# Optimization experiments

Hardware: AMD Instinct MI355X
Metric: run time of the kernel (lower is better)

The kernel has to match this reference:

```python
import jax, jax.numpy as jnp
import numpy as np

# ---- instant-ngp style multi-resolution hash-grid config (matches torch-ngp HashEncoder) ----
NUM_LEVELS = 16
LEVEL_DIM = 2
BASE_RES = 16
DESIRED_RES = 2048
LOG2_T = 19
T_MAX = 2 ** LOG2_T
_pls = np.exp2(np.log2(DESIRED_RES / BASE_RES) / (NUM_LEVELS - 1))  # per-level scale ~1.3819
RESOLUTIONS = [int(np.ceil(BASE_RES * _pls ** l)) for l in range(NUM_LEVELS)]
LEVEL_SIZES = [min(T_MAX, int(np.ceil((r + 1) ** 3 / 8) * 8)) for r in RESOLUTIONS]
OFFSETS = np.concatenate([[0], np.cumsum(LEVEL_SIZES)]).astype(np.int64)
TOTAL_PARAMS = int(OFFSETS[-1])
HASHED = [(r + 1) ** 3 > T_MAX for r in RESOLUTIONS]
CORNERS = np.array([[i, j, k] for i in (0, 1) for j in (0, 1) for k in (0, 1)], dtype=np.float32)  # [8,3]

N_POINTS = 524288
MULTIRES = 6  # positional embedding freqs -> input_ch = 3 + 3*2*6 = 39
D_IN0 = 3 + MULTIRES * 6 + NUM_LEVELS * LEVEL_DIM  # 71


def hash_encode(x, table):
    """x: [N,3] in [0,1]; table: [TOTAL_PARAMS, LEVEL_DIM] -> [N, NUM_LEVELS*LEVEL_DIM]."""
    cn = jnp.asarray(CORNERS)              # [8,3]
    cn_u = cn.astype(jnp.uint32)
    p1, p2, p3 = jnp.uint32(1), jnp.uint32(2654435761), jnp.uint32(805459861)
    outs = []
    for l in range(NUM_LEVELS):
        res = RESOLUTIONS[l]
        pos = x * jnp.float32(res - 1)     # [N,3]
        p0 = jnp.floor(pos)
        w = pos - p0                        # [N,3] trilinear fractions
        cpos = p0.astype(jnp.uint32)[:, None, :] + cn_u[None]  # [N,8,3] corner coords
        if HASHED[l]:
            idx = (cpos[..., 0] * p1) ^ (cpos[..., 1] * p2) ^ (cpos[..., 2] * p3)
            idx = (idx % jnp.uint32(LEVEL_SIZES[l])).astype(jnp.int32)
        else:
            stride = jnp.uint32(res + 1)
            idx = (cpos[..., 0] + cpos[..., 1] * stride + cpos[..., 2] * stride * stride).astype(jnp.int32)
        feats = table[int(OFFSETS[l]) + idx]  # [N,8,LEVEL_DIM] irregular gather
        cw = jnp.where(cn[None] == 1.0, w[:, None, :], 1.0 - w[:, None, :])  # [N,8,3]
        wgt = cw[..., 0] * cw[..., 1] * cw[..., 2]  # [N,8]
        outs.append(jnp.einsum('nc,ncd->nd', wgt, feats))  # [N,LEVEL_DIM]
    return jnp.concatenate(outs, axis=-1)


def pos_embed(x):
    # NeRF embedder, include_input=True, log-sampled freqs 2^0..2^(MULTIRES-1), sin/cos
    freqs = jnp.asarray(2.0 ** np.arange(MULTIRES), dtype=x.dtype)   # [6]
    ang = x[:, None, :] * freqs[None, :, None]                        # [N,6,3]
    sc = jnp.stack([jnp.sin(ang), jnp.cos(ang)], axis=2)              # [N,6,2,3]
    return jnp.concatenate([x, sc.reshape(x.shape[0], -1)], axis=-1)  # [N,39]


def linear_wn(x, v, g, b):
    # nn.utils.weight_norm: W = g * v / ||v||_row
    Wn = v * (g / jnp.linalg.norm(v, axis=1))[:, None]
    return x @ Wn.T + b


def softplus100(x):
    # nn.Softplus(beta=100)
    return jax.nn.softplus(100.0 * x) * 0.01


def setup_inputs() -> dict:
    key = jax.random.key(0)
    ks = jax.random.split(key, 8)
    x = jax.random.uniform(ks[0], (N_POINTS, 3), dtype=jnp.float32)
    hash_table = jax.random.uniform(ks[1], (TOTAL_PARAMS, LEVEL_DIM), jnp.float32, -1e-4, 1e-4)

    def lin(k, dout, din):
        v = jax.random.normal(k, (dout, din), jnp.float32) * jnp.float32(np.sqrt(2.0 / dout))
        g = jnp.linalg.norm(v, axis=1)  # weight_norm init: g = ||v||
        b = jnp.zeros((dout,), jnp.float32)
        return v, g, b

    v0, g0, b0 = lin(ks[2], 256, D_IN0)   # 71 -> 256
    v1, g1, b1 = lin(ks[3], 256, 256)     # 256 -> 256
    v2, g2, b2 = lin(ks[4], 257, 256)     # 256 -> 1 + feature_vector_size
    return {"x": x, "hash_table": hash_table,
            "v0": v0, "g0": g0, "b0": b0,
            "v1": v1, "g1": g1, "b1": b1,
            "v2": v2, "g2": g2, "b2": b2}


def reference(x, hash_table, v0, g0, b0, v1, g1, b1, v2, g2, b2):
    # ImplicitNetworkGrid.forward (divide_factor = 1.0, use_grid_feature = True)
    feat = hash_encode(x, hash_table)                    # [N,32]
    h = jnp.concatenate([pos_embed(x), feat], axis=-1)   # [N,71] = cat(embed, feature)
    h = softplus100(linear_wn(h, v0, g0, b0))
    h = softplus100(linear_wn(h, v1, g1, b1))
    return linear_wn(h, v2, g2, b2)                      # [N,257]: sdf + feature vector
```

## Files before the change

### kernel.cpp

```cpp
#include <hip/hip_runtime.h>
#include <cmath>

typedef float f32x4 __attribute__((ext_vector_type(4)));
typedef short short8 __attribute__((ext_vector_type(8)));

#define N_POINTS 524288
#define TMASK 0x7FFFFu

struct HashCfg { int res[16]; int off[16]; unsigned hashed_mask; int total; };

#define S0_OFF   0
#define S1_OFF   1024
#define S2_OFF   2048
#define W2L_OFF  3328
#define B0_OFF   4608
#define B1_OFF   (B0_OFF + 49152)
#define B2_OFF   (B1_OFF + 131072)
#define TBF_OFF  (B2_OFF + 131072)

__device__ inline unsigned short f2bf(float f){
  unsigned u = __float_as_uint(f);
  u = (u + 0x7FFFu + ((u >> 16) & 1u)) >> 16;
  return (unsigned short)u;
}
__device__ inline float bf2f(unsigned short h){
  return __uint_as_float(((unsigned)h) << 16);
}
__device__ inline float softplus100_fast(float x){
  float y = 100.f * x;
  return 0.01f * (fmaxf(y, 0.f) + __logf(1.f + __expf(-fabsf(y))));
}

__global__ void scale_kernel(const float* __restrict__ v0, const float* __restrict__ g0,
                             const float* __restrict__ v1, const float* __restrict__ g1,
                             const float* __restrict__ v2, const float* __restrict__ g2,
                             char* __restrict__ ws){
  int r = blockIdx.x * 256 + threadIdx.x;
  if (r < 256){
    float s = 0.f;
    for (int k = 0; k < 71; k++){ float t = v0[r*71+k]; s += t*t; }
    ((float*)(ws + S0_OFF))[r] = g0[r] / sqrtf(s);
  } else if (r < 512){
    int o = r - 256; float s = 0.f;
    for (int k = 0; k < 256; k++){ float t = v1[o*256+k]; s += t*t; }
    ((float*)(ws + S1_OFF))[o] = g1[o] / sqrtf(s);
  } else if (r < 769){
    int o = r - 512; float s = 0.f;
    for (int k = 0; k < 256; k++){ float t = v2[o*256+k]; s += t*t; }
    ((float*)(ws + S2_OFF))[o] = g2[o] / sqrtf(s);
  }
}

__global__ void pack_kernel(const float* __restrict__ v0, const float* __restrict__ v1,
                            const float* __restrict__ v2, char* __restrict__ ws){
  int i = blockIdx.x * 256 + threadIdx.x;
  const float* s0 = (const float*)(ws + S0_OFF);
  const float* s1 = (const float*)(ws + S1_OFF);
  const float* s2 = (const float*)(ws + S2_OFF);
  if (i < 24576){
    int j = i & 7, l = (i >> 3) & 63, q = i >> 9;
    int kt = q % 3, nt = q / 3;
    int k = kt*32 + (l >> 4)*8 + j, col = nt*16 + (l & 15);
    float v = (k < 71) ? v0[col*71 + k] * s0[col] : 0.f;
    ((unsigned short*)(ws + B0_OFF))[i] = f2bf(v);
  } else if (i < 90112){
    int e = i - 24576;
    int j = e & 7, l = (e >> 3) & 63, q = e >> 9;
    int kt = q & 7, nt = q >> 3;
    int k = kt*32 + (l >> 4)*8 + j, col = nt*16 + (l & 15);
    ((unsigned short*)(ws + B1_OFF))[e] = f2bf(v1[col*256 + k] * s1[col]);
  } else if (i < 155648){
    int e = i - 90112;
    int j = e & 7, l = (e >> 3) & 63, q = e >> 9;
    int kt = q & 7, nt = q >> 3;
    int k = kt*32 + (l >> 4)*8 + j, col = nt*16 + (l & 15);
    ((unsigned short*)(ws + B2_OFF))[e] = f2bf(v2[col*256 + k] * s2[col]);
  } else if (i < 155904){
    int k = i - 155648;
    ((float*)(ws + W2L_OFF))[k] = v2[256*256 + k] * s2[256];
  }
}

__global__ void tconv_kernel(const float* __restrict__ table, char* __restrict__ ws, int total){
  int i = blockIdx.x * 256 + threadIdx.x;
  if (i < total){
    float2 v = ((const float2*)table)[i];
    unsigned lo = ((unsigned)f2bf(v.x));
    unsigned hi = ((unsigned)f2bf(v.y)) << 16;
    ((unsigned*)(ws + TBF_OFF))[i] = lo | hi;
  }
}

template<int USEBF>
__global__ __launch_bounds__(256, 4) void fused2(
    const float* __restrict__ xin, const float* __restrict__ table,
    char* __restrict__ ws,
    const float* __restrict__ b0, const float* __restrict__ b1, const float* __restrict__ b2,
    float* __restrict__ out, HashCfg cfg)
{
  __shared__ unsigned short buf[64 * 256];
  __shared__ float colsc[4][64];

  const int tid = threadIdx.x;
  const int p   = tid & 63;
  const int grp = tid >> 6;
  const int gp  = blockIdx.x * 64 + p;

  const float x0 = xin[gp*3], x1 = xin[gp*3+1], x2 = xin[gp*3+2];
  const unsigned* __restrict__ tbf = (const unsigned*)(ws + TBF_OFF);

  auto stB = [&](int row, int col, float v){
    buf[row*256 + (col ^ ((row & 7) << 3))] = f2bf(v);
  };
  auto ldB = [&](int row, int kb) -> short8 {
    return *(const short8*)&buf[row*256 + (kb ^ ((row & 7) << 3))];
  };

  {
    float wxa[4], wya[4], wza[4];
    unsigned vb[2][8];
    float2   vf2[2][8];

    auto issue_level = [&](int ii, int slot){
      int lev = grp*4 + ii;
      int res = cfg.res[lev];
      float scl = (float)(res - 1);
      float px = x0*scl, py = x1*scl, pz = x2*scl;
      float fx = floorf(px), fy = floorf(py), fz = floorf(pz);
      wxa[ii] = px - fx; wya[ii] = py - fy; wza[ii] = pz - fz;
      unsigned cx0 = (unsigned)fx, cy0 = (unsigned)fy, cz0 = (unsigned)fz;
      unsigned r1 = (unsigned)(res + 1);
      bool hl = (cfg.hashed_mask >> lev) & 1;
      unsigned base = (unsigned)cfg.off[lev];
      #pragma unroll
      for (int c = 0; c < 8; c++){
        unsigned bx = (c >> 2) & 1, by = (c >> 1) & 1, bz = c & 1;
        unsigned cx = cx0 + bx, cy = cy0 + by, cz = cz0 + bz;
        unsigned idx = hl ? ((cx ^ (cy * 2654435761u) ^ (cz * 805459861u)) & TMASK)
                          : (cx + cy * r1 + cz * r1 * r1);
        if (USEBF) vb[slot][c]  = tbf[base + idx];
        else       vf2[slot][c] = *(const float2*)(table + (size_t)(base + idx) * 2u);
      }
    };
    auto consume_level = [&](int ii, int slot){
      int lev = grp*4 + ii;
      float wx = wxa[ii], wy = wya[ii], wz = wza[ii];
      float f0 = 0.f, f1 = 0.f;
      #pragma unroll
      for (int c = 0; c < 8; c++){
        unsigned bx = (c >> 2) & 1, by = (c >> 1) & 1, bz = c & 1;
        float w = (bx ? wx : 1.f - wx) * (by ? wy : 1.f - wy) * (bz ? wz : 1.f - wz);
        if (USEBF){
          unsigned u = vb[slot][c];
          f0 += w * __uint_as_float(u << 16);
          f1 += w * __uint_as_float(u & 0xffff0000u);
        } else {
          f0 += w * vf2[slot][c].x;
          f1 += w * vf2[slot][c].y;
        }
      }
      stB(p, 39 + 2*lev, f0);
      stB(p, 40 + 2*lev, f1);
    };

    issue_level(0, 0); issue_level(1, 1);

    if (grp < 3){
      float xv[3] = {x0, x1, x2};
      #pragma unroll
      for (int fi = 0; fi < 2; fi++){
        int f = grp*2 + fi;
        float fr = (float)(1 << f);
        #pragma unroll
        for (int d = 0; d < 3; d++){
          float a = xv[d] * fr;
          stB(p, 3 + f*6 + d,     __sinf(a));
          stB(p, 3 + f*6 + 3 + d, __cosf(a));
        }
      }
    } else {
      stB(p, 0, x0); stB(p, 1, x1); stB(p, 2, x2);
      #pragma unroll
      for (int c = 71; c < 96; c++)
        buf[p*256 + (c ^ ((p & 7) << 3))] = 0;
    }

    consume_level(0, 0); consume_level(1, 1);
    issue_level(2, 0);   issue_level(3, 1);
    consume_level(2, 0); consume_level(3, 1);
  }
  __syncthreads();

  const int l  = tid & 63;
  const int lr = l & 15;
  const int lh = l >> 4;
  const int wv = grp;
  const short8* B0p = (const short8*)(ws + B0_OFF);
  const short8* B1p = (const short8*)(ws + B1_OFF);
  const short8* B2p = (const short8*)(ws + B2_OFF);

  {
    f32x4 acc[4][4];
    #pragma unroll
    for (int a = 0; a < 4; a++)
      #pragma unroll
      for (int b = 0; b < 4; b++) acc[a][b] = (f32x4){0.f,0.f,0.f,0.f};
    #pragma unroll
    for (int kt = 0; kt < 3; kt++){
      short8 af[4];
      #pragma unroll
      for (int mt = 0; mt < 4; mt++) af[mt] = ldB(mt*16 + lr, kt*32 + lh*8);
      #pragma unroll
      for (int nt = 0; nt < 4; nt++){
        short8 bf = B0p[((wv*4 + nt)*3 + kt)*64 + l];
        #pragma unroll
        for (int mt = 0; mt < 4; mt++)
          acc[mt][nt] = __builtin_amdgcn_mfma_f32_16x16x32_bf16(af[mt], bf, acc[mt][nt], 0, 0, 0);
      }
    }
    __syncthreads();
    float bb[4];
    #pragma unroll
    for (int nt = 0; nt < 4; nt++) bb[nt] = b0[wv*64 + nt*16 + lr];
    #pragma unroll
    for (int mt = 0; mt < 4; mt++)
      #pragma unroll
      for (int nt = 0; nt < 4; nt++){
        int c = wv*64 + nt*16 + lr;
        #pragma unroll
        for (int j = 0; j < 4; j++)
          stB(mt*16 + lh*4 + j, c, softplus100_fast(acc[mt][nt][j] + bb[nt]));
      }
  }
  __syncthreads();

  {
    f32x4 acc[4][4];
    #pragma unroll
    for (int a = 0; a < 4; a++)
      #pragma unroll
      for (int b = 0; b < 4; b++) acc[a][b] = (f32x4){0.f,0.f,0.f,0.f};
    #pragma unroll
    for (int kt = 0; kt < 8; kt++){
      short8 af[4];
      #pragma unroll
      for (int mt = 0; mt < 4; mt++) af[mt] = ldB(mt*16 + lr, kt*32 + lh*8);
      #pragma unroll
      for (int nt = 0; nt < 4; nt++){
        short8 bf = B1p[((wv*4 + nt)*8 + kt)*64 + l];
        #pragma unroll
        for (int mt = 0; mt < 4; mt++)
          acc[mt][nt] = __builtin_amdgcn_mfma_f32_16x16x32_bf16(af[mt], bf, acc[mt][nt], 0, 0, 0);
      }
    }
    __syncthreads();
    float bb[4];
    #pragma unroll
    for (int nt = 0; nt < 4; nt++) bb[nt] = b1[wv*64 + nt*16 + lr];
    #pragma unroll
    for (int mt = 0; mt < 4; mt++)
      #pragma unroll
      for (int nt = 0; nt < 4; nt++){
        int c = wv*64 + nt*16 + lr;
        #pragma unroll
        for (int j = 0; j < 4; j++)
          stB(mt*16 + lh*4 + j, c, softplus100_fast(acc[mt][nt][j] + bb[nt]));
      }
  }
  __syncthreads();

  {
    const float* w2l = (const float*)(ws + W2L_OFF);
    float s = 0.f;
    #pragma unroll
    for (int q = 0; q < 8; q++){
      short8 h = ldB(l, wv*64 + q*8);
      #pragma unroll
      for (int j = 0; j < 8; j++)
        s += bf2f((unsigned short)h[j]) * w2l[wv*64 + q*8 + j];
    }
    colsc[wv][l] = s;
  }

  {
    f32x4 acc[4][4];
    #pragma unroll
    for (int a = 0; a < 4; a++)
      #pragma unroll
      for (int b = 0; b < 4; b++) acc[a][b] = (f32x4){0.f,0.f,0.f,0.f};
    #pragma unroll
    for (int kt = 0; kt < 8; kt++){
      short8 af[4];
      #pragma unroll
      for (int mt = 0; mt < 4; mt++) af[mt] = ldB(mt*16 + lr, kt*32 + lh*8);
      #pragma unroll
      for (int nt = 0; nt < 4; nt++){
        short8 bf = B2p[((wv*4 + nt)*8 + kt)*64 + l];
        #pragma unroll
        for (int mt = 0; mt < 4; mt++)
          acc[mt][nt] = __builtin_amdgcn_mfma_f32_16x16x32_bf16(af[mt], bf, acc[mt][nt], 0, 0, 0);
      }
    }
    float bb[4];
    #pragma unroll
    for (int nt = 0; nt < 4; nt++) bb[nt] = b2[wv*64 + nt*16 + lr];
    const float b2last = b2[256];

    float* st = (float*)buf;
    #pragma unroll
    for (int r16 = 0; r16 < 4; r16++){
      __syncthreads();
      #pragma unroll
      for (int nt = 0; nt < 4; nt++){
        int c = wv*64 + nt*16 + lr;
        #pragma unroll
        for (int j = 0; j < 4; j++)
          st[(lh*4 + j)*257 + c] = acc[r16][nt][j] + bb[nt];
      }
      if (tid < 16){
        int gr = r16*16 + tid;
        st[tid*257 + 256] = colsc[0][gr] + colsc[1][gr] + colsc[2][gr] + colsc[3][gr] + b2last;
      }
      __syncthreads();
      float4* dst4 = (float4*)(out + (size_t)(blockIdx.x*64 + r16*16) * 257);
      const float4* src4 = (const float4*)st;
      #pragma unroll 5
      for (int i = tid; i < 1028; i += 256) dst4[i] = src4[i];
    }
  }
}

static HashCfg make_cfg(){
  HashCfg c;
  double pls = exp2(log2(2048.0 / 16.0) / 15.0);
  long long off = 0;
  unsigned mask = 0;
  for (int l = 0; l < 16; l++){
    int r = (int)ceil(16.0 * pow(pls, (double)l));
    c.res[l] = r;
    c.off[l] = (int)off;
    double n3 = (double)(r + 1) * (double)(r + 1) * (double)(r + 1);
    long long size;
    if (n3 > 524288.0){ mask |= (1u << l); }
    size = (long long)(ceil(n3 / 8.0) * 8.0);
    if (size > 524288) size = 524288;
    off += size;
  }
  c.hashed_mask = mask;
  c.total = (int)off;
  return c;
}

extern "C" void kernel_launch(void* const* d_in, const int* in_sizes, int n_in,
                              void* d_out, int out_size, void* d_ws, size_t ws_size,
                              hipStream_t stream) {
  const float* x     = (const float*)d_in[0];
  const float* table = (const float*)d_in[1];
  const float* v0 = (const float*)d_in[2];
  const float* g0 = (const float*)d_in[3];
  const float* b0 = (const float*)d_in[4];
  const float* v1 = (const float*)d_in[5];
  const float* g1 = (const float*)d_in[6];
  const float* b1 = (const float*)d_in[7];
  const float* v2 = (const float*)d_in[8];
  const float* g2 = (const float*)d_in[9];
  const float* b2 = (const float*)d_in[10];
  float* out = (float*)d_out;
  char* ws = (char*)d_ws;

  HashCfg cfg = make_cfg();
  size_t ws_need_bf = (size_t)TBF_OFF + (size_t)cfg.total * 4u;

  hipLaunchKernelGGL(scale_kernel, dim3(4), dim3(256), 0, stream, v0, g0, v1, g1, v2, g2, ws);
  hipLaunchKernelGGL(pack_kernel, dim3(609), dim3(256), 0, stream, v0, v1, v2, ws);

  if (ws_size >= ws_need_bf){
    hipLaunchKernelGGL(tconv_kernel, dim3((cfg.total + 255) / 256), dim3(256), 0, stream,
                       table, ws, cfg.total);
    hipLaunchKernelGGL((fused2<1>), dim3(N_POINTS / 64), dim3(256), 0, stream,
                       x, table, ws, b0, b1, b2, out, cfg);
  } else {
    hipLaunchKernelGGL((fused2<0>), dim3(N_POINTS / 64), dim3(256), 0, stream,
                       x, table, ws, b0, b1, b2, out, cfg);
  }
}
```

Measured before the change: 870.2 us.

## Sort points by Morton cell before fused hash-grid MLP to improve gather locality

Adds a counting sort of points by a 32^3 Morton-coded cell (histogram, single-block scan, atomic scatter), so each block processes spatially nearby points. The goal is better cache reuse in the hash-table gathers. Blocks are remapped with an XCD-style swizzle, and all four levels' gathers are now issued before any are consumed. The output is written directly to permuted rows instead of being staged through shared memory for coalesced float4 stores. The trade-offs are three extra kernels plus a memset, uncoalesced scattered output writes of 257-float rows, and more registers held live for the gathers.

```diff
diff --git a/kernel.cpp b/kernel.cpp
--- a/kernel.cpp
+++ b/kernel.cpp
@@ -6,6 +6,7 @@
 
 #define N_POINTS 524288
 #define TMASK 0x7FFFFu
+#define NCELLS 32768
 
 struct HashCfg { int res[16]; int off[16]; unsigned hashed_mask; int total; };
 
@@ -29,6 +30,16 @@
 __device__ inline float softplus100_fast(float x){
   float y = 100.f * x;
   return 0.01f * (fmaxf(y, 0.f) + __logf(1.f + __expf(-fabsf(y))));
+}
+__device__ inline unsigned morton5(unsigned cx, unsigned cy, unsigned cz){
+  unsigned k = 0;
+  #pragma unroll
+  for (int b = 0; b < 5; b++){
+    k |= ((cx >> b) & 1u) << (3*b)
+       | ((cy >> b) & 1u) << (3*b + 1)
+       | ((cz >> b) & 1u) << (3*b + 2);
+  }
+  return k;
 }
 
 __global__ void scale_kernel(const float* __restrict__ v0, const float* __restrict__ g0,
@@ -91,22 +102,66 @@
   }
 }
 
+__global__ void hist_kernel(const float* __restrict__ xin,
+                            unsigned* __restrict__ hist, unsigned* __restrict__ keys){
+  int i = blockIdx.x * 256 + threadIdx.x;
+  float x0 = xin[i*3], x1 = xin[i*3+1], x2 = xin[i*3+2];
+  unsigned cx = min(31u, (unsigned)(x0 * 32.f));
+  unsigned cy = min(31u, (unsigned)(x1 * 32.f));
+  unsigned cz = min(31u, (unsigned)(x2 * 32.f));
+  unsigned k = morton5(cx, cy, cz);
+  keys[i] = k;
+  atomicAdd(&hist[k], 1u);
+}
+
+__global__ __launch_bounds__(1024) void scan_kernel(unsigned* __restrict__ hist){
+  __shared__ unsigned sdata[1024];
+  int t = threadIdx.x;
+  unsigned loc[32];
+  unsigned s = 0;
+  #pragma unroll
+  for (int k = 0; k < 32; k++){ loc[k] = hist[t*32 + k]; s += loc[k]; }
+  sdata[t] = s;
+  __syncthreads();
+  for (int d = 1; d < 1024; d <<= 1){
+    unsigned v = (t >= d) ? sdata[t - d] : 0u;
+    __syncthreads();
+    sdata[t] += v;
+    __syncthreads();
+  }
+  unsigned run = (t == 0) ? 0u : sdata[t - 1];
+  #pragma unroll
+  for (int k = 0; k < 32; k++){ unsigned c = loc[k]; hist[t*32 + k] = run; run += c; }
+}
+
+__global__ void scatter_kernel(const unsigned* __restrict__ keys,
+                               unsigned* __restrict__ hist, int* __restrict__ perm){
+  int i = blockIdx.x * 256 + threadIdx.x;
+  unsigned k = keys[i];
+  unsigned r = atomicAdd(&hist[k], 1u);
+  perm[r] = i;
+}
+
 template<int USEBF>
-__global__ __launch_bounds__(256, 4) void fused2(
+__global__ __launch_bounds__(256, 4) void fused3(
     const float* __restrict__ xin, const float* __restrict__ table,
-    char* __restrict__ ws,
+    char* __restrict__ ws, const int* __restrict__ perm,
     const float* __restrict__ b0, const float* __restrict__ b1, const float* __restrict__ b2,
     float* __restrict__ out, HashCfg cfg)
 {
   __shared__ unsigned short buf[64 * 256];
   __shared__ float colsc[4][64];
+  __shared__ int pids[64];
 
   const int tid = threadIdx.x;
   const int p   = tid & 63;
   const int grp = tid >> 6;
-  const int gp  = blockIdx.x * 64 + p;
-
-  const float x0 = xin[gp*3], x1 = xin[gp*3+1], x2 = xin[gp*3+2];
+  const int lb  = (blockIdx.x & 7) * 1024 + (blockIdx.x >> 3);
+  const int idx = lb * 64 + p;
+  const int pid = perm ? perm[idx] : idx;
+  if (grp == 0) pids[p] = pid;
+
+  const float x0 = xin[pid*3], x1 = xin[pid*3+1], x2 = xin[pid*3+2];
   const unsigned* __restrict__ tbf = (const unsigned*)(ws + TBF_OFF);
 
   auto stB = [&](int row, int col, float v){
@@ -118,10 +173,11 @@
 
   {
     float wxa[4], wya[4], wza[4];
-    unsigned vb[2][8];
-    float2   vf2[2][8];
-
-    auto issue_level = [&](int ii, int slot){
+    unsigned vb[4][8];
+    float2   vf2[4][8];
+
+    #pragma unroll
+    for (int ii = 0; ii < 4; ii++){
       int lev = grp*4 + ii;
       int res = cfg.res[lev];
       float scl = (float)(res - 1);
@@ -136,34 +192,12 @@
       for (int c = 0; c < 8; c++){
         unsigned bx = (c >> 2) & 1, by = (c >> 1) & 1, bz = c & 1;
         unsigned cx = cx0 + bx, cy = cy0 + by, cz = cz0 + bz;
-        unsigned idx = hl ? ((cx ^ (cy * 2654435761u) ^ (cz * 805459861u)) & TMASK)
-                          : (cx + cy * r1 + cz * r1 * r1);
-        if (USEBF) vb[slot][c]  = tbf[base + idx];
-        else       vf2[slot][c] = *(const float2*)(table + (size_t)(base + idx) * 2u);
-      }
-    };
-    auto consume_level = [&](int ii, int slot){
-      int lev = grp*4 + ii;
-      float wx = wxa[ii], wy = wya[ii], wz = wza[ii];
-      float f0 = 0.f, f1 = 0.f;
-      #pragma unroll
-      for (int c = 0; c < 8; c++){
-        unsigned bx = (c >> 2) & 1, by = (c >> 1) & 1, bz = c & 1;
-        float w = (bx ? wx : 1.f - wx) * (by ? wy : 1.f - wy) * (bz ? wz : 1.f - wz);
-        if (USEBF){
-          unsigned u = vb[slot][c];
-          f0 += w * __uint_as_float(u << 16);
-          f1 += w * __uint_as_float(u & 0xffff0000u);
-        } else {
-          f0 += w * vf2[slot][c].x;
-          f1 += w * vf2[slot][c].y;
-        }
-      }
-      stB(p, 39 + 2*lev, f0);
-      stB(p, 40 + 2*lev, f1);
-    };
-
-    issue_level(0, 0); issue_level(1, 1);
+        unsigned hidx = hl ? ((cx ^ (cy * 2654435761u) ^ (cz * 805459861u)) & TMASK)
+                           : (cx + cy * r1 + cz * r1 * r1);
+        if (USEBF) vb[ii][c]  = tbf[base + hidx];
+        else       vf2[ii][c] = *(const float2*)(table + (size_t)(base + hidx) * 2u);
+      }
+    }
 
     if (grp < 3){
       float xv[3] = {x0, x1, x2};
@@ -185,9 +219,27 @@
         buf[p*256 + (c ^ ((p & 7) << 3))] = 0;
     }
 
-    consume_level(0, 0); consume_level(1, 1);
-    issue_level(2, 0);   issue_level(3, 1);
-    consume_level(2, 0); consume_level(3, 1);
+    #pragma unroll
+    for (int ii = 0; ii < 4; ii++){
+      int lev = grp*4 + ii;
+      float wx = wxa[ii], wy = wya[ii], wz = wza[ii];
+      float f0 = 0.f, f1 = 0.f;
+      #pragma unroll
+      for (int c = 0; c < 8; c++){
+        unsigned bx = (c >> 2) & 1, by = (c >> 1) & 1, bz = c & 1;
+        float w = (bx ? wx : 1.f - wx) * (by ? wy : 1.f - wy) * (bz ? wz : 1.f - wz);
+        if (USEBF){
+          unsigned u = vb[ii][c];
+          f0 += w * __uint_as_float(u << 16);
+          f1 += w * __uint_as_float(u & 0xffff0000u);
+        } else {
+          f0 += w * vf2[ii][c].x;
+          f1 += w * vf2[ii][c].y;
+        }
+      }
+      stB(p, 39 + 2*lev, f0);
+      stB(p, 40 + 2*lev, f1);
+    }
   }
   __syncthreads();
 
@@ -301,32 +353,27 @@
           acc[mt][nt] = __builtin_amdgcn_mfma_f32_16x16x32_bf16(af[mt], bf, acc[mt][nt], 0, 0, 0);
       }
     }
+    __syncthreads();
     float bb[4];
     #pragma unroll
     for (int nt = 0; nt < 4; nt++) bb[nt] = b2[wv*64 + nt*16 + lr];
-    const float b2last = b2[256];
-
-    float* st = (float*)buf;
-    #pragma unroll
-    for (int r16 = 0; r16 < 4; r16++){
-      __syncthreads();
+    int rowid[4][4];
+    #pragma unroll
+    for (int mt = 0; mt < 4; mt++)
+      #pragma unroll
+      for (int j = 0; j < 4; j++) rowid[mt][j] = pids[mt*16 + lh*4 + j];
+    #pragma unroll
+    for (int mt = 0; mt < 4; mt++)
       #pragma unroll
       for (int nt = 0; nt < 4; nt++){
         int c = wv*64 + nt*16 + lr;
         #pragma unroll
         for (int j = 0; j < 4; j++)
-          st[(lh*4 + j)*257 + c] = acc[r16][nt][j] + bb[nt];
-      }
-      if (tid < 16){
-        int gr = r16*16 + tid;
-        st[tid*257 + 256] = colsc[0][gr] + colsc[1][gr] + colsc[2][gr] + colsc[3][gr] + b2last;
-      }
-      __syncthreads();
-      float4* dst4 = (float4*)(out + (size_t)(blockIdx.x*64 + r16*16) * 257);
-      const float4* src4 = (const float4*)st;
-      #pragma unroll 5
-      for (int i = tid; i < 1028; i += 256) dst4[i] = src4[i];
-    }
+          out[(size_t)rowid[mt][j]*257 + c] = acc[mt][nt][j] + bb[nt];
+      }
+    if (tid < 64)
+      out[(size_t)pids[tid]*257 + 256] =
+        colsc[0][tid] + colsc[1][tid] + colsc[2][tid] + colsc[3][tid] + b2[256];
   }
 }
 
@@ -369,18 +416,35 @@
   char* ws = (char*)d_ws;
 
   HashCfg cfg = make_cfg();
-  size_t ws_need_bf = (size_t)TBF_OFF + (size_t)cfg.total * 4u;
+  size_t tbf_bytes = (size_t)cfg.total * 4u;
+  size_t hist_off  = (TBF_OFF + tbf_bytes + 255) & ~(size_t)255;
+  size_t keys_off  = hist_off + (size_t)NCELLS * 4;
+  size_t perm_off  = keys_off + (size_t)N_POINTS * 4;
+  size_t need_sort = perm_off + (size_t)N_POINTS * 4;
+  size_t need_bf   = TBF_OFF + tbf_bytes;
 
   hipLaunchKernelGGL(scale_kernel, dim3(4), dim3(256), 0, stream, v0, g0, v1, g1, v2, g2, ws);
   hipLaunchKernelGGL(pack_kernel, dim3(609), dim3(256), 0, stream, v0, v1, v2, ws);
 
-  if (ws_size >= ws_need_bf){
+  if (ws_size >= need_sort){
+    unsigned* hist = (unsigned*)(ws + hist_off);
+    unsigned* keys = (unsigned*)(ws + keys_off);
+    int*      perm = (int*)(ws + perm_off);
+    hipMemsetAsync(hist, 0, (size_t)NCELLS * 4, stream);
     hipLaunchKernelGGL(tconv_kernel, dim3((cfg.total + 255) / 256), dim3(256), 0, stream,
                        table, ws, cfg.total);
-    hipLaunchKernelGGL((fused2<1>), dim3(N_POINTS / 64), dim3(256), 0, stream,
-                       x, table, ws, b0, b1, b2, out, cfg);
+    hipLaunchKernelGGL(hist_kernel, dim3(N_POINTS / 256), dim3(256), 0, stream, x, hist, keys);
+    hipLaunchKernelGGL(scan_kernel, dim3(1), dim3(1024), 0, stream, hist);
+    hipLaunchKernelGGL(scatter_kernel, dim3(N_POINTS / 256), dim3(256), 0, stream, keys, hist, perm);
+    hipLaunchKernelGGL((fused3<1>), dim3(N_POINTS / 64), dim3(256), 0, stream,
+                       x, table, ws, perm, b0, b1, b2, out, cfg);
+  } else if (ws_size >= need_bf){
+    hipLaunchKernelGGL(tconv_kernel, dim3((cfg.total + 255) / 256), dim3(256), 0, stream,
+                       table, ws, cfg.total);
+    hipLaunchKernelGGL((fused3<1>), dim3(N_POINTS / 64), dim3(256), 0, stream,
+                       x, table, ws, (const int*)nullptr, b0, b1, b2, out, cfg);
   } else {
-    hipLaunchKernelGGL((fused2<0>), dim3(N_POINTS / 64), dim3(256), 0, stream,
-                       x, table, ws, b0, b1, b2, out, cfg);
-  }
-}
+    hipLaunchKernelGGL((fused3<0>), dim3(N_POINTS / 64), dim3(256), 0, stream,
+                       x, table, ws, (const int*)nullptr, b0, b1, b2, out, cfg);
+  }
+}
```

Measured after the change: 789.1 us. 9.3% less time.
